# Kernel optimization log

Hardware: AMD Instinct MI355X
Metric: run time of the kernel (lower is better)

## Reference

```python
import jax, jax.numpy as jnp
import numpy as np

B, Q, K, D, H, HD, OUT = 4, 1024, 1024, 256, 8, 32, 256


def setup_inputs() -> dict:
    key = jax.random.key(0)
    ks = jax.random.split(key, 11)
    s = 0.05  # small init scale for weights
    return {
        "q_data": jax.random.normal(ks[0], (B, Q, D), jnp.float32),
        "m_data": jax.random.normal(ks[1], (B, K, D), jnp.float32),
        "bias": jax.random.normal(ks[2], (B, 1, 1, K), jnp.float32),
        "nonbatched_bias": jax.random.normal(ks[3], (H, Q, K), jnp.float32),
        "query_w": jax.random.normal(ks[4], (D, H, HD), jnp.float32) * s,
        "key_w": jax.random.normal(ks[5], (D, H, HD), jnp.float32) * s,
        "value_w": jax.random.normal(ks[6], (D, H, HD), jnp.float32) * s,
        "gating_w": jax.random.normal(ks[7], (D, H, HD), jnp.float32) * s,
        "gating_b": jnp.ones((H, HD), jnp.float32),
        "output_w": jax.random.normal(ks[8], (H, HD, OUT), jnp.float32) * s,
        "output_b": jnp.zeros((OUT,), jnp.float32),
    }


def reference(q_data, m_data, bias, nonbatched_bias, query_w, key_w, value_w,
              gating_w, gating_b, output_w, output_b):
    key_dim = query_w.shape[-1]
    # QKV projections; queries pre-scaled by 1/sqrt(head_dim)
    q = jnp.einsum('bqa,ahc->bqhc', q_data, query_w) * key_dim ** (-0.5)
    k = jnp.einsum('bka,ahc->bkhc', m_data, key_w)
    v = jnp.einsum('bka,ahc->bkhc', m_data, value_w)
    # attention logits [b,h,q,k] plus batched and nonbatched additive biases
    logits_update = jnp.einsum('bqhc,bkhc->bhqk', q, k)
    logits = logits_update + bias + nonbatched_bias[None]
    weights = jax.nn.softmax(logits, axis=-1)
    weighted_avg = jnp.einsum('bhqk,bkhc->bqhc', weights, v)
    # sigmoid gating on the value-aggregated output
    gate = jax.nn.sigmoid(jnp.einsum('bqc,chv->bqhv', q_data, gating_w) + gating_b)
    weighted_avg = weighted_avg * gate
    output = jnp.einsum('bqhc,hco->bqo', weighted_avg, output_w) + output_b
    return (output, logits_update)
```

## Files before the change

kernel.cpp:

```cpp
#include <hip/hip_runtime.h>
#include <hip/hip_bf16.h>

#define NB 4
#define NQ 1024
#define NKS 1024
#define ND 256
#define NH 8
#define NHD 32
#define NOUT 256
#define SPLIT 4

typedef __attribute__((ext_vector_type(8))) short v8s;
typedef __attribute__((ext_vector_type(4))) short v4s;
typedef __attribute__((ext_vector_type(4))) float f32x4;

__global__ __launch_bounds__(256) void prep_all(
    const float* __restrict__ qd, const float* __restrict__ md,
    const float* __restrict__ qw, const float* __restrict__ kw,
    const float* __restrict__ vw, const float* __restrict__ gw,
    const float* __restrict__ ow,
    __hip_bfloat16* __restrict__ Abf, __hip_bfloat16* __restrict__ Wt)
{
  if (blockIdx.x < 1024) {
    const int gid = blockIdx.x * 256 + threadIdx.x;
    const float* src = (gid < 131072) ? qd : md;
    const size_t off = (size_t)(gid & 131071) * 8;
    const float4 a = ((const float4*)(src + off))[0];
    const float4 c = ((const float4*)(src + off))[1];
    __hip_bfloat16 t8[8];
    t8[0]=__float2bfloat16(a.x); t8[1]=__float2bfloat16(a.y);
    t8[2]=__float2bfloat16(a.z); t8[3]=__float2bfloat16(a.w);
    t8[4]=__float2bfloat16(c.x); t8[5]=__float2bfloat16(c.y);
    t8[6]=__float2bfloat16(c.z); t8[7]=__float2bfloat16(c.w);
    *(v8s*)(Abf + (size_t)gid * 8) = *(v8s*)t8;
    return;
  }
  __shared__ float tile[64][65];
  const int wb = blockIdx.x - 1024;
  const int m = wb >> 4, bx = wb & 15;
  const float* src = (m == 0) ? qw : (m == 1) ? kw : (m == 2) ? vw
                   : (m == 3) ? gw : ow;
  const float scale = (m == 0) ? 0.1767766952966369f : 1.0f;
  const int d0 = (bx >> 2) * 64, o0 = (bx & 3) * 64;
  #pragma unroll
  for (int i = 0; i < 16; ++i) {
    const int idx = threadIdx.x + i * 256;
    tile[idx >> 6][idx & 63] = src[(size_t)(d0 + (idx >> 6)) * 256 + o0 + (idx & 63)];
  }
  __syncthreads();
  __hip_bfloat16* dst = Wt + (size_t)m * 65536;
  #pragma unroll
  for (int i = 0; i < 16; ++i) {
    const int idx = threadIdx.x + i * 256;
    const int orow = idx >> 6, dc = idx & 63;
    dst[(size_t)(o0 + orow) * 256 + d0 + dc] = __float2bfloat16(tile[dc][orow] * scale);
  }
}

__global__ __launch_bounds__(256) void proj_kernel(
    const __hip_bfloat16* __restrict__ Abf, const __hip_bfloat16* __restrict__ Wt,
    const float* __restrict__ gating_b,
    __hip_bfloat16* __restrict__ Qw, __hip_bfloat16* __restrict__ Kw,
    __hip_bfloat16* __restrict__ Vt, float* __restrict__ G)
{
  const int wv = threadIdx.x >> 6, lane = threadIdx.x & 63;
  const int c = lane & 15, g = lane >> 4;
  const int task = blockIdx.x * 4 + wv;
  const int ctg = task & 3;
  const int mat = (task >> 2) & 1;
  const int r0g = (task >> 3) & 255;
  const int src = task >> 11;
  const int r0 = r0g * 16;
  const int b = r0 >> 10, pos0 = r0 & 1023;
  const f32x4 z = {0.f, 0.f, 0.f, 0.f};

  const __hip_bfloat16* A = Abf + ((size_t)src * 4096 + r0) * 256;
  v8s af[8];
  #pragma unroll
  for (int ks = 0; ks < 8; ++ks)
    af[ks] = *(const v8s*)(A + c * 256 + ks * 32 + g * 8);

  const int widx = (src == 0) ? (mat ? 3 : 0) : (mat ? 2 : 1);
  const __hip_bfloat16* W = Wt + (size_t)widx * 65536;
  const bool swapped = (src == 1) && (mat == 1);

  f32x4 ac[4] = {z, z, z, z};
  #pragma unroll
  for (int ks = 0; ks < 8; ++ks) {
    #pragma unroll
    for (int j = 0; j < 4; ++j) {
      v8s wf = *(const v8s*)(W + (size_t)((ctg * 4 + j) * 16 + c) * 256 + ks * 32 + g * 8);
      ac[j] = swapped
        ? __builtin_amdgcn_mfma_f32_16x16x32_bf16(wf, af[ks], ac[j], 0, 0, 0)
        : __builtin_amdgcn_mfma_f32_16x16x32_bf16(af[ks], wf, ac[j], 0, 0, 0);
    }
  }

  if (src == 0 && mat == 0) {
    #pragma unroll
    for (int j = 0; j < 4; ++j) {
      const int o = (ctg * 4 + j) * 16 + c, h = o >> 5, hd = o & 31;
      #pragma unroll
      for (int r = 0; r < 4; ++r)
        Qw[((size_t)(b * NH + h) * 1024 + pos0 + 4 * g + r) * 32 + hd] =
            __float2bfloat16(ac[j][r]);
    }
  } else if (src == 0) {
    #pragma unroll
    for (int j = 0; j < 4; ++j) {
      const int o = (ctg * 4 + j) * 16 + c;
      const float gb = gating_b[o];
      #pragma unroll
      for (int r = 0; r < 4; ++r)
        G[(size_t)(r0 + 4 * g + r) * 256 + o] = ac[j][r] + gb;
    }
  } else if (mat == 0) {
    #pragma unroll
    for (int j = 0; j < 4; ++j) {
      const int o = (ctg * 4 + j) * 16 + c, h = o >> 5, hd = o & 31;
      #pragma unroll
      for (int r = 0; r < 4; ++r)
        Kw[((size_t)(b * NH + h) * 1024 + pos0 + 4 * g + r) * 32 + hd] =
            __float2bfloat16(ac[j][r]);
    }
  } else {
    #pragma unroll
    for (int j = 0; j < 4; ++j) {
      #pragma unroll
      for (int r = 0; r < 4; ++r) {
        const int o2 = (ctg * 4 + j) * 16 + 4 * g + r;
        Vt[((size_t)(b * NH + (o2 >> 5)) * 32 + (o2 & 31)) * 1024 + pos0 + c] =
            __float2bfloat16(ac[j][r]);
      }
    }
  }
}

__global__ __launch_bounds__(256) void attn_kernel(
    const __hip_bfloat16* __restrict__ Qw, const __hip_bfloat16* __restrict__ Kw,
    const __hip_bfloat16* __restrict__ Vt,
    const float* __restrict__ bias, const float* __restrict__ nbb,
    float* __restrict__ out_logits,
    __hip_bfloat16* __restrict__ partO, float* __restrict__ partL)
{
  __shared__ __align__(16) __hip_bfloat16 sP[4][16][72];

  const int wv = threadIdx.x >> 6, lane = threadIdx.x & 63;
  const int c = lane & 15, g = lane >> 4;
  const int xcd   = blockIdx.x & 7;
  const int slot  = blockIdx.x >> 3;
  const int bh    = ((slot >> 6) << 3) | xcd;
  const int inner = slot & 63;
  const int sp    = inner >> 4;
  const int qtg   = inner & 15;
  const int qt  = qtg * 4 + wv;
  const int b = bh >> 3, h = bh & 7;
  const int rem = bh * 64 + qt;
  const int q0 = qt * 16;
  const int kbase = sp * (NKS / SPLIT);
  const size_t bhs = (size_t)bh;

  const __hip_bfloat16* Kbase = Kw + bhs * NKS * NHD;
  const __hip_bfloat16* Vbase = Vt + bhs * NHD * NKS;
  const float* biasb = bias + (size_t)b * NKS;
  const float* nbbb  = nbb + ((size_t)h * NQ + q0) * NKS;

  const v8s qfrag = *(const v8s*)(Qw + (bhs * NQ + q0 + c) * NHD + g * 8);

  const f32x4 zacc = {0.f, 0.f, 0.f, 0.f};
  f32x4 O0 = zacc, O1 = zacc;
  float lsumL[4] = {0.f, 0.f, 0.f, 0.f};

  auto loadKV = [&](int k0, v8s* kf, v8s* vf) {
    kf[0] = *(const v8s*)(Kbase + (k0 +      c) * NHD + g * 8);
    kf[1] = *(const v8s*)(Kbase + (k0 + 16 + c) * NHD + g * 8);
    kf[2] = *(const v8s*)(Kbase + (k0 + 32 + c) * NHD + g * 8);
    kf[3] = *(const v8s*)(Kbase + (k0 + 48 + c) * NHD + g * 8);
    vf[0] = *(const v8s*)(Vbase + (     c) * NKS + k0 +      g * 8);
    vf[1] = *(const v8s*)(Vbase + (16 + c) * NKS + k0 +      g * 8);
    vf[2] = *(const v8s*)(Vbase + (     c) * NKS + k0 + 32 + g * 8);
    vf[3] = *(const v8s*)(Vbase + (16 + c) * NKS + k0 + 32 + g * 8);
  };
  auto loadBias = [&](int k0, float* bn) {
    #pragma unroll
    for (int t = 0; t < 4; ++t) {
      const float bvt = biasb[k0 + t * 16 + c];
      #pragma unroll
      for (int r = 0; r < 4; ++r)
        bn[t * 4 + r] = bvt + nbbb[(g * 4 + r) * NKS + k0 + t * 16 + c];
    }
  };

  auto compute = [&](int k0, const v8s* kf, const v8s* vf, const float* bn) {
    f32x4 S[4];
    #pragma unroll
    for (int t = 0; t < 4; ++t)
      S[t] = __builtin_amdgcn_mfma_f32_16x16x32_bf16(qfrag, kf[t], zacc, 0, 0, 0);

    #pragma unroll
    for (int r = 0; r < 4; ++r) {
      const int qrow = q0 + g * 4 + r;
      float* lp = out_logits + (bhs * NQ + qrow) * (size_t)NKS + k0 + c;
      float psum = 0.f;
      #pragma unroll
      for (int t = 0; t < 4; ++t) {
        lp[t * 16] = S[t][r];
        const float p = __expf(S[t][r] + bn[t * 4 + r]);
        psum += p;
        sP[wv][g * 4 + r][t * 16 + c] = __float2bfloat16(p);
      }
      lsumL[r] += psum;
    }

    const v8s pa0 = *(const v8s*)&sP[wv][c][g * 8];
    const v8s pa1 = *(const v8s*)&sP[wv][c][32 + g * 8];
    O0 = __builtin_amdgcn_mfma_f32_16x16x32_bf16(pa0, vf[0], O0, 0, 0, 0);
    O0 = __builtin_amdgcn_mfma_f32_16x16x32_bf16(pa1, vf[2], O0, 0, 0, 0);
    O1 = __builtin_amdgcn_mfma_f32_16x16x32_bf16(pa0, vf[1], O1, 0, 0, 0);
    O1 = __builtin_amdgcn_mfma_f32_16x16x32_bf16(pa1, vf[3], O1, 0, 0, 0);
  };

  v8s kfA[4], vfA[4], kfB[4], vfB[4];
  float bnA[16], bnB[16];

  loadKV(kbase, kfA, vfA);
  loadBias(kbase, bnA);
  #pragma unroll 1
  for (int kt = 0; kt < NKS / SPLIT / 64; kt += 2) {
    loadKV(kbase + (kt + 1) * 64, kfB, vfB);
    loadBias(kbase + (kt + 1) * 64, bnB);
    compute(kbase + kt * 64, kfA, vfA, bnA);
    if (kt + 2 < NKS / SPLIT / 64) {
      loadKV(kbase + (kt + 2) * 64, kfA, vfA);
      loadBias(kbase + (kt + 2) * 64, bnA);
    }
    compute(kbase + (kt + 1) * 64, kfB, vfB, bnB);
  }

  #pragma unroll
  for (int r = 0; r < 4; ++r) {
    float rs = lsumL[r];
    rs += __shfl_xor(rs, 1);
    rs += __shfl_xor(rs, 2);
    rs += __shfl_xor(rs, 4);
    rs += __shfl_xor(rs, 8);
    const int row = 4 * g + r;
    const size_t pb = ((size_t)(rem * SPLIT + sp) * 16 + row) * 32;
    partO[pb + c]      = __float2bfloat16(O0[r]);
    partO[pb + 16 + c] = __float2bfloat16(O1[r]);
    if (c == 0) partL[(size_t)(rem * SPLIT + sp) * 16 + row] = rs;
  }
}

__global__ __launch_bounds__(256) void outproj_kernel(
    const __hip_bfloat16* __restrict__ partO, const float* __restrict__ partL,
    const float* __restrict__ G, const __hip_bfloat16* __restrict__ WtO,
    const float* __restrict__ output_b, float* __restrict__ out)
{
  __shared__ __align__(16) __hip_bfloat16 sRows[16][264];
  const int t = threadIdx.x;
  const int wv = t >> 6, lane = t & 63;
  const int c = lane & 15, g = lane >> 4;
  const int r0 = blockIdx.x * 16;
  const int b = r0 >> 10, qt = (r0 & 1023) >> 4;
  const int h = t >> 5, hd = t & 31;
  const int rem = (b * NH + h) * 64 + qt;

  #pragma unroll 4
  for (int row = 0; row < 16; ++row) {
    float o = 0.f, l = 0.f;
    #pragma unroll
    for (int sp = 0; sp < SPLIT; ++sp) {
      const size_t base = (size_t)(rem * SPLIT + sp) * 16 + row;
      o += __bfloat162float(partO[base * 32 + hd]);
      l += partL[base];
    }
    const float gl = G[(size_t)(r0 + row) * 256 + t];
    sRows[row][t] = __float2bfloat16((o / l) * (1.f / (1.f + __expf(-gl))));
  }
  __syncthreads();

  const f32x4 z = {0.f, 0.f, 0.f, 0.f};
  f32x4 ac[4] = {z, z, z, z};
  #pragma unroll
  for (int ks = 0; ks < 8; ++ks) {
    const v8s af = *(const v8s*)&sRows[c][ks * 32 + g * 8];
    #pragma unroll
    for (int j = 0; j < 4; ++j) {
      const v8s wf = *(const v8s*)(WtO + (size_t)((wv * 4 + j) * 16 + c) * 256 + ks * 32 + g * 8);
      ac[j] = __builtin_amdgcn_mfma_f32_16x16x32_bf16(af, wf, ac[j], 0, 0, 0);
    }
  }
  #pragma unroll
  for (int j = 0; j < 4; ++j) {
    const int o = (wv * 4 + j) * 16 + c;
    const float ob = output_b[o];
    #pragma unroll
    for (int r = 0; r < 4; ++r)
      out[(size_t)(r0 + 4 * g + r) * 256 + o] = ac[j][r] + ob;
  }
}

extern "C" void kernel_launch(void* const* d_in, const int* in_sizes, int n_in,
                              void* d_out, int out_size, void* d_ws, size_t ws_size,
                              hipStream_t stream) {
  const float* q_data   = (const float*)d_in[0];
  const float* m_data   = (const float*)d_in[1];
  const float* bias     = (const float*)d_in[2];
  const float* nbb      = (const float*)d_in[3];
  const float* query_w  = (const float*)d_in[4];
  const float* key_w    = (const float*)d_in[5];
  const float* value_w  = (const float*)d_in[6];
  const float* gating_w = (const float*)d_in[7];
  const float* gating_b = (const float*)d_in[8];
  const float* output_w = (const float*)d_in[9];
  const float* output_b = (const float*)d_in[10];

  float* out        = (float*)d_out;
  float* out_logits = out + (size_t)NB * NQ * NOUT;

  char* ws = (char*)d_ws;
  const size_t MB = 1u << 20;
  __hip_bfloat16* Qw  = (__hip_bfloat16*)(ws);
  __hip_bfloat16* Kw  = (__hip_bfloat16*)(ws + 2 * MB);
  __hip_bfloat16* Vt  = (__hip_bfloat16*)(ws + 4 * MB);
  float*          G   = (float*)(ws + 6 * MB);
  __hip_bfloat16* Abf = (__hip_bfloat16*)(ws + 10 * MB);
  __hip_bfloat16* partO = (__hip_bfloat16*)(ws + 10 * MB);
  float*          partL = (float*)(ws + 19 * MB);
  __hip_bfloat16* Wt  = (__hip_bfloat16*)(ws + 20 * MB);

  prep_all<<<1104, 256, 0, stream>>>(q_data, m_data, query_w, key_w, value_w,
                                     gating_w, output_w, Abf, Wt);
  proj_kernel<<<1024, 256, 0, stream>>>(Abf, Wt, gating_b, Qw, Kw, Vt, G);
  attn_kernel<<<2048, 256, 0, stream>>>(Qw, Kw, Vt, bias, nbb, out_logits, partO, partL);
  outproj_kernel<<<256, 256, 0, stream>>>(partO, partL, G, Wt + (size_t)4 * 65536,
                                          output_b, out);
}
```

Before: 85.28 us.

## Process two query tiles per wave in attention and split output projection columns

Each wave in the attention kernel now handles 32 query rows (two 16-row tiles) instead of 16, so every loaded K/V fragment feeds twice as many MFMAs. This halves K/V global traffic per query and halves the attention grid. It also raises register pressure (double bias buffers and accumulators), which may lower occupancy. Separately, the output projection is split across two blocks per 16-row tile by output-column half, doubling that grid for more parallelism but recomputing the gated row staging in both blocks.

```diff
diff --git a/kernel.cpp b/kernel.cpp
--- a/kernel.cpp
+++ b/kernel.cpp
@@ -143,33 +143,36 @@
     float* __restrict__ out_logits,
     __hip_bfloat16* __restrict__ partO, float* __restrict__ partL)
 {
-  __shared__ __align__(16) __hip_bfloat16 sP[4][16][72];
+  __shared__ __align__(16) __hip_bfloat16 sP[4][2][16][72];
 
   const int wv = threadIdx.x >> 6, lane = threadIdx.x & 63;
   const int c = lane & 15, g = lane >> 4;
   const int xcd   = blockIdx.x & 7;
   const int slot  = blockIdx.x >> 3;
-  const int bh    = ((slot >> 6) << 3) | xcd;
-  const int inner = slot & 63;
-  const int sp    = inner >> 4;
-  const int qtg   = inner & 15;
-  const int qt  = qtg * 4 + wv;
+  const int bh    = ((slot >> 5) << 3) | xcd;
+  const int inner = slot & 31;
+  const int sp    = inner >> 3;
+  const int qpg   = inner & 7;
+  const int qp    = qpg * 4 + wv;
+  const int q0    = qp * 32;
   const int b = bh >> 3, h = bh & 7;
-  const int rem = bh * 64 + qt;
-  const int q0 = qt * 16;
   const int kbase = sp * (NKS / SPLIT);
   const size_t bhs = (size_t)bh;
+  const int rem0 = bh * 64 + qp * 2;
+  const int rem1 = rem0 + 1;
 
   const __hip_bfloat16* Kbase = Kw + bhs * NKS * NHD;
   const __hip_bfloat16* Vbase = Vt + bhs * NHD * NKS;
   const float* biasb = bias + (size_t)b * NKS;
   const float* nbbb  = nbb + ((size_t)h * NQ + q0) * NKS;
 
-  const v8s qfrag = *(const v8s*)(Qw + (bhs * NQ + q0 + c) * NHD + g * 8);
+  const v8s qf0 = *(const v8s*)(Qw + (bhs * NQ + q0 + c) * NHD + g * 8);
+  const v8s qf1 = *(const v8s*)(Qw + (bhs * NQ + q0 + 16 + c) * NHD + g * 8);
 
   const f32x4 zacc = {0.f, 0.f, 0.f, 0.f};
-  f32x4 O0 = zacc, O1 = zacc;
-  float lsumL[4] = {0.f, 0.f, 0.f, 0.f};
+  f32x4 O00 = zacc, O01 = zacc, O10 = zacc, O11 = zacc;
+  float ls0[4] = {0.f, 0.f, 0.f, 0.f};
+  float ls1[4] = {0.f, 0.f, 0.f, 0.f};
 
   auto loadKV = [&](int k0, v8s* kf, v8s* vf) {
     kf[0] = *(const v8s*)(Kbase + (k0 +      c) * NHD + g * 8);
@@ -181,74 +184,110 @@
     vf[2] = *(const v8s*)(Vbase + (     c) * NKS + k0 + 32 + g * 8);
     vf[3] = *(const v8s*)(Vbase + (16 + c) * NKS + k0 + 32 + g * 8);
   };
-  auto loadBias = [&](int k0, float* bn) {
-    #pragma unroll
-    for (int t = 0; t < 4; ++t) {
-      const float bvt = biasb[k0 + t * 16 + c];
-      #pragma unroll
-      for (int r = 0; r < 4; ++r)
-        bn[t * 4 + r] = bvt + nbbb[(g * 4 + r) * NKS + k0 + t * 16 + c];
+  auto loadBias = [&](int k0, float* bn0, float* bn1) {
+    #pragma unroll
+    for (int t4 = 0; t4 < 4; ++t4) {
+      const float bvt = biasb[k0 + t4 * 16 + c];
+      #pragma unroll
+      for (int r = 0; r < 4; ++r) {
+        bn0[t4 * 4 + r] = bvt + nbbb[(size_t)(g * 4 + r) * NKS + k0 + t4 * 16 + c];
+        bn1[t4 * 4 + r] = bvt + nbbb[(size_t)(16 + g * 4 + r) * NKS + k0 + t4 * 16 + c];
+      }
     }
   };
 
-  auto compute = [&](int k0, const v8s* kf, const v8s* vf, const float* bn) {
-    f32x4 S[4];
-    #pragma unroll
-    for (int t = 0; t < 4; ++t)
-      S[t] = __builtin_amdgcn_mfma_f32_16x16x32_bf16(qfrag, kf[t], zacc, 0, 0, 0);
+  auto compute = [&](int k0, const v8s* kf, const v8s* vf,
+                     const float* bn0, const float* bn1) {
+    f32x4 S0[4], S1[4];
+    #pragma unroll
+    for (int t4 = 0; t4 < 4; ++t4) {
+      S0[t4] = __builtin_amdgcn_mfma_f32_16x16x32_bf16(qf0, kf[t4], zacc, 0, 0, 0);
+      S1[t4] = __builtin_amdgcn_mfma_f32_16x16x32_bf16(qf1, kf[t4], zacc, 0, 0, 0);
+    }
 
     #pragma unroll
     for (int r = 0; r < 4; ++r) {
-      const int qrow = q0 + g * 4 + r;
-      float* lp = out_logits + (bhs * NQ + qrow) * (size_t)NKS + k0 + c;
-      float psum = 0.f;
-      #pragma unroll
-      for (int t = 0; t < 4; ++t) {
-        lp[t * 16] = S[t][r];
-        const float p = __expf(S[t][r] + bn[t * 4 + r]);
-        psum += p;
-        sP[wv][g * 4 + r][t * 16 + c] = __float2bfloat16(p);
+      float* lp = out_logits + (bhs * NQ + q0 + g * 4 + r) * (size_t)NKS + k0 + c;
+      float ps = 0.f;
+      #pragma unroll
+      for (int t4 = 0; t4 < 4; ++t4) {
+        lp[t4 * 16] = S0[t4][r];
+        const float p = __expf(S0[t4][r] + bn0[t4 * 4 + r]);
+        ps += p;
+        sP[wv][0][g * 4 + r][t4 * 16 + c] = __float2bfloat16(p);
       }
-      lsumL[r] += psum;
-    }
-
-    const v8s pa0 = *(const v8s*)&sP[wv][c][g * 8];
-    const v8s pa1 = *(const v8s*)&sP[wv][c][32 + g * 8];
-    O0 = __builtin_amdgcn_mfma_f32_16x16x32_bf16(pa0, vf[0], O0, 0, 0, 0);
-    O0 = __builtin_amdgcn_mfma_f32_16x16x32_bf16(pa1, vf[2], O0, 0, 0, 0);
-    O1 = __builtin_amdgcn_mfma_f32_16x16x32_bf16(pa0, vf[1], O1, 0, 0, 0);
-    O1 = __builtin_amdgcn_mfma_f32_16x16x32_bf16(pa1, vf[3], O1, 0, 0, 0);
+      ls0[r] += ps;
+    }
+    #pragma unroll
+    for (int r = 0; r < 4; ++r) {
+      float* lp = out_logits + (bhs * NQ + q0 + 16 + g * 4 + r) * (size_t)NKS + k0 + c;
+      float ps = 0.f;
+      #pragma unroll
+      for (int t4 = 0; t4 < 4; ++t4) {
+        lp[t4 * 16] = S1[t4][r];
+        const float p = __expf(S1[t4][r] + bn1[t4 * 4 + r]);
+        ps += p;
+        sP[wv][1][g * 4 + r][t4 * 16 + c] = __float2bfloat16(p);
+      }
+      ls1[r] += ps;
+    }
+
+    const v8s pa00 = *(const v8s*)&sP[wv][0][c][g * 8];
+    const v8s pa01 = *(const v8s*)&sP[wv][0][c][32 + g * 8];
+    const v8s pa10 = *(const v8s*)&sP[wv][1][c][g * 8];
+    const v8s pa11 = *(const v8s*)&sP[wv][1][c][32 + g * 8];
+    O00 = __builtin_amdgcn_mfma_f32_16x16x32_bf16(pa00, vf[0], O00, 0, 0, 0);
+    O00 = __builtin_amdgcn_mfma_f32_16x16x32_bf16(pa01, vf[2], O00, 0, 0, 0);
+    O01 = __builtin_amdgcn_mfma_f32_16x16x32_bf16(pa00, vf[1], O01, 0, 0, 0);
+    O01 = __builtin_amdgcn_mfma_f32_16x16x32_bf16(pa01, vf[3], O01, 0, 0, 0);
+    O10 = __builtin_amdgcn_mfma_f32_16x16x32_bf16(pa10, vf[0], O10, 0, 0, 0);
+    O10 = __builtin_amdgcn_mfma_f32_16x16x32_bf16(pa11, vf[2], O10, 0, 0, 0);
+    O11 = __builtin_amdgcn_mfma_f32_16x16x32_bf16(pa10, vf[1], O11, 0, 0, 0);
+    O11 = __builtin_amdgcn_mfma_f32_16x16x32_bf16(pa11, vf[3], O11, 0, 0, 0);
   };
 
   v8s kfA[4], vfA[4], kfB[4], vfB[4];
-  float bnA[16], bnB[16];
+  float bn0A[16], bn1A[16], bn0B[16], bn1B[16];
 
   loadKV(kbase, kfA, vfA);
-  loadBias(kbase, bnA);
+  loadBias(kbase, bn0A, bn1A);
   #pragma unroll 1
   for (int kt = 0; kt < NKS / SPLIT / 64; kt += 2) {
     loadKV(kbase + (kt + 1) * 64, kfB, vfB);
-    loadBias(kbase + (kt + 1) * 64, bnB);
-    compute(kbase + kt * 64, kfA, vfA, bnA);
+    loadBias(kbase + (kt + 1) * 64, bn0B, bn1B);
+    compute(kbase + kt * 64, kfA, vfA, bn0A, bn1A);
     if (kt + 2 < NKS / SPLIT / 64) {
       loadKV(kbase + (kt + 2) * 64, kfA, vfA);
-      loadBias(kbase + (kt + 2) * 64, bnA);
-    }
-    compute(kbase + (kt + 1) * 64, kfB, vfB, bnB);
+      loadBias(kbase + (kt + 2) * 64, bn0A, bn1A);
+    }
+    compute(kbase + (kt + 1) * 64, kfB, vfB, bn0B, bn1B);
   }
 
   #pragma unroll
   for (int r = 0; r < 4; ++r) {
-    float rs = lsumL[r];
+    float rs = ls0[r];
     rs += __shfl_xor(rs, 1);
     rs += __shfl_xor(rs, 2);
     rs += __shfl_xor(rs, 4);
     rs += __shfl_xor(rs, 8);
     const int row = 4 * g + r;
-    const size_t pb = ((size_t)(rem * SPLIT + sp) * 16 + row) * 32;
-    partO[pb + c]      = __float2bfloat16(O0[r]);
-    partO[pb + 16 + c] = __float2bfloat16(O1[r]);
-    if (c == 0) partL[(size_t)(rem * SPLIT + sp) * 16 + row] = rs;
+    const size_t pb = ((size_t)(rem0 * SPLIT + sp) * 16 + row) * 32;
+    partO[pb + c]      = __float2bfloat16(O00[r]);
+    partO[pb + 16 + c] = __float2bfloat16(O01[r]);
+    if (c == 0) partL[(size_t)(rem0 * SPLIT + sp) * 16 + row] = rs;
+  }
+  #pragma unroll
+  for (int r = 0; r < 4; ++r) {
+    float rs = ls1[r];
+    rs += __shfl_xor(rs, 1);
+    rs += __shfl_xor(rs, 2);
+    rs += __shfl_xor(rs, 4);
+    rs += __shfl_xor(rs, 8);
+    const int row = 4 * g + r;
+    const size_t pb = ((size_t)(rem1 * SPLIT + sp) * 16 + row) * 32;
+    partO[pb + c]      = __float2bfloat16(O10[r]);
+    partO[pb + 16 + c] = __float2bfloat16(O11[r]);
+    if (c == 0) partL[(size_t)(rem1 * SPLIT + sp) * 16 + row] = rs;
   }
 }
 
@@ -261,7 +300,8 @@
   const int t = threadIdx.x;
   const int wv = t >> 6, lane = t & 63;
   const int c = lane & 15, g = lane >> 4;
-  const int r0 = blockIdx.x * 16;
+  const int r0 = (blockIdx.x >> 1) * 16;
+  const int colh = blockIdx.x & 1;
   const int b = r0 >> 10, qt = (r0 & 1023) >> 4;
   const int h = t >> 5, hd = t & 31;
   const int rem = (b * NH + h) * 64 + qt;
@@ -281,19 +321,20 @@
   __syncthreads();
 
   const f32x4 z = {0.f, 0.f, 0.f, 0.f};
-  f32x4 ac[4] = {z, z, z, z};
+  f32x4 ac[2] = {z, z};
   #pragma unroll
   for (int ks = 0; ks < 8; ++ks) {
     const v8s af = *(const v8s*)&sRows[c][ks * 32 + g * 8];
     #pragma unroll
-    for (int j = 0; j < 4; ++j) {
-      const v8s wf = *(const v8s*)(WtO + (size_t)((wv * 4 + j) * 16 + c) * 256 + ks * 32 + g * 8);
+    for (int j = 0; j < 2; ++j) {
+      const int o = colh * 128 + (wv * 2 + j) * 16 + c;
+      const v8s wf = *(const v8s*)(WtO + (size_t)o * 256 + ks * 32 + g * 8);
       ac[j] = __builtin_amdgcn_mfma_f32_16x16x32_bf16(af, wf, ac[j], 0, 0, 0);
     }
   }
   #pragma unroll
-  for (int j = 0; j < 4; ++j) {
-    const int o = (wv * 4 + j) * 16 + c;
+  for (int j = 0; j < 2; ++j) {
+    const int o = colh * 128 + (wv * 2 + j) * 16 + c;
     const float ob = output_b[o];
     #pragma unroll
     for (int r = 0; r < 4; ++r)
@@ -333,7 +374,7 @@
   prep_all<<<1104, 256, 0, stream>>>(q_data, m_data, query_w, key_w, value_w,
                                      gating_w, output_w, Abf, Wt);
   proj_kernel<<<1024, 256, 0, stream>>>(Abf, Wt, gating_b, Qw, Kw, Vt, G);
-  attn_kernel<<<2048, 256, 0, stream>>>(Qw, Kw, Vt, bias, nbb, out_logits, partO, partL);
-  outproj_kernel<<<256, 256, 0, stream>>>(partO, partL, G, Wt + (size_t)4 * 65536,
+  attn_kernel<<<1024, 256, 0, stream>>>(Qw, Kw, Vt, bias, nbb, out_logits, partO, partL);
+  outproj_kernel<<<512, 256, 0, stream>>>(partO, partL, G, Wt + (size_t)4 * 65536,
                                           output_b, out);
 }
```

Measured after the change: 91.22 us. +7.0%, slower.
